# Kernel optimization log

Hardware: AMD Instinct MI355X
Metric: run time of the kernel (lower is better)

The kernel has to match this reference:

```python
import jax, jax.numpy as jnp
import numpy as np

N = 50000   # n_nodes (== input_dim, featureless identity features)
E = 800000  # edges per support (avg degree 16)
D = 200     # embed_dim (hardcoded in GIN)
C = 10      # num_classes


def setup_inputs() -> dict:
    key = jax.random.key(0)
    ks = jax.random.split(key, 8)
    x = jnp.zeros((N, 1), jnp.float32)  # unused: layer 0 is featureless
    rows0 = jax.random.randint(ks[0], (E,), 0, N, dtype=jnp.int32)
    cols0 = jax.random.randint(ks[1], (E,), 0, N, dtype=jnp.int32)
    vals0 = jax.random.uniform(ks[2], (E,), jnp.float32)
    rows1 = jax.random.randint(ks[3], (E,), 0, N, dtype=jnp.int32)
    cols1 = jax.random.randint(ks[4], (E,), 0, N, dtype=jnp.int32)
    vals1 = jax.random.uniform(ks[5], (E,), jnp.float32)
    W0 = jax.random.normal(ks[6], (N, D), jnp.float32) * 0.02
    W1 = jax.random.normal(ks[7], (D, C), jnp.float32) * 0.05
    eps0 = jnp.zeros((1,), jnp.float32)  # train_eps init (~1e-4 in repo)
    eps1 = jnp.zeros((1,), jnp.float32)
    return dict(x=x, rows0=rows0, cols0=cols0, vals0=vals0,
                rows1=rows1, cols1=cols1, vals1=vals1,
                W0=W0, W1=W1, eps0=eps0, eps1=eps1)


def reference(x, rows0, cols0, vals0, rows1, cols1, vals1, W0, W1, eps0, eps1):
    # sparse A @ X via gather + segment-sum (A in COO: rows, cols, vals)
    def spmm(r, c, v, X):
        return jax.ops.segment_sum(v[:, None] * X[c], r, num_segments=N)

    # Layer 0 (featureless, num_mlp_layers==1):
    #   AX = sum_i A_i ; out = AX @ W0 + 0.1*(1+eps0)*W0
    h0 = spmm(rows0, cols0, vals0, W0) + spmm(rows1, cols1, vals1, W0) \
         + 0.1 * (1.0 + eps0[0]) * W0
    h = jax.nn.relu(h0)  # [N, D]

    # Layer 1 (with features): out = (sum_i A_i @ h + 0.1*(1+eps1)*h) @ W1
    ax = spmm(rows0, cols0, vals0, h) + spmm(rows1, cols1, vals1, h)
    out = (ax + 0.1 * (1.0 + eps1[0]) * h) @ W1  # [N, C]
    return out
```

## Files before the change

kernel.cpp:

```cpp
#include <hip/hip_runtime.h>

#define N_NODES 50000
#define E_EDGES 800000
#define E2      (2 * E_EDGES)
#define D_DIM   200
#define C_CLS   10
#define NB_SCAN   ((N_NODES + 255) / 256)
#define NB_BUCKET ((N_NODES + 255) / 256)
#define BATCH     4096
#define CAP       12288

static __device__ __forceinline__ unsigned short f2bf(float f) {
    unsigned u = __float_as_uint(f);
    return (unsigned short)((u + 0x7FFFu + ((u >> 16) & 1u)) >> 16);
}
static __device__ __forceinline__ float bf_lo(unsigned u) {
    return __uint_as_float(u << 16);
}
static __device__ __forceinline__ float bf_hi(unsigned u) {
    return __uint_as_float(u & 0xFFFF0000u);
}

__global__ __launch_bounds__(256) void convert_w0_kernel(const float* __restrict__ W0,
                                                         unsigned short* __restrict__ W0h,
                                                         int* __restrict__ bcur) {
    if (blockIdx.x == 0 && threadIdx.x < NB_BUCKET) bcur[threadIdx.x] = 0;
    int i = (blockIdx.x * 256 + threadIdx.x) * 4;
    if (i >= N_NODES * D_DIM) return;
    float4 f = *(const float4*)(W0 + i);
    uint2 p;
    p.x = (unsigned)f2bf(f.x) | ((unsigned)f2bf(f.y) << 16);
    p.y = (unsigned)f2bf(f.z) | ((unsigned)f2bf(f.w) << 16);
    *(uint2*)(W0h + i) = p;
}

__global__ __launch_bounds__(256) void bucket_scatter_kernel(
        const int* __restrict__ rows0, const int* __restrict__ cols0,
        const float* __restrict__ vals0,
        const int* __restrict__ rows1, const int* __restrict__ cols1,
        const float* __restrict__ vals1,
        int* __restrict__ bcur,
        int2* __restrict__ stage) {
    __shared__ int cntL[NB_BUCKET];
    __shared__ int baseL[NB_BUCKET];
    __shared__ int offL[NB_BUCKET];
    __shared__ int2 recL[BATCH];
    const int tid = threadIdx.x;
    const int e0 = blockIdx.x * BATCH;

    for (int b = tid; b < NB_BUCKET; b += 256) cntL[b] = 0;
    __syncthreads();

#pragma unroll
    for (int k = 0; k < BATCH / 256; ++k) {
        int idx = k * 256 + tid;
        int e = e0 + idx;
        if (e < E2) {
            int r, c;
            float v;
            if (e < E_EDGES) {
                r = rows0[e]; c = cols0[e]; v = vals0[e];
            } else {
                int e1 = e - E_EDGES;
                r = rows1[e1]; c = cols1[e1]; v = vals1[e1];
            }
            recL[idx] = make_int2((int)((unsigned)r | ((unsigned)c << 16)),
                                  __float_as_int(v));
            atomicAdd(&cntL[r >> 8], 1);
        }
    }
    __syncthreads();

    for (int b = tid; b < NB_BUCKET; b += 256) {
        int c = cntL[b];
        baseL[b] = (c > 0) ? atomicAdd(&bcur[b], c) : 0;
        offL[b] = 0;
    }
    __syncthreads();

#pragma unroll
    for (int k = 0; k < BATCH / 256; ++k) {
        int idx = k * 256 + tid;
        int e = e0 + idx;
        if (e < E2) {
            int2 rec = recL[idx];
            int b = (int)(((unsigned)rec.x & 0xFFFFu) >> 8);
            int pos = baseL[b] + atomicAdd(&offL[b], 1);
            stage[(size_t)b * CAP + pos] = rec;
        }
    }
}

__global__ __launch_bounds__(256) void row_count_kernel(const int* __restrict__ bcur,
                                                        const int2* __restrict__ stage,
                                                        int* __restrict__ cnt) {
    __shared__ int hist[256];
    const int b = blockIdx.x;
    const int tid = threadIdx.x;
    hist[tid] = 0;
    __syncthreads();

    const int n = bcur[b];
    const int2* __restrict__ sp = stage + (size_t)b * CAP;
    for (int i = tid; i < n; i += 256)
        atomicAdd(&hist[(unsigned)sp[i].x & 255u], 1);
    __syncthreads();

    const int row = (b << 8) + tid;
    if (row < N_NODES) cnt[row] = hist[tid];
}

__global__ __launch_bounds__(256) void scan1_kernel(const int* __restrict__ cnt,
                                                    int* __restrict__ incl,
                                                    int* __restrict__ bsum) {
    const int i = blockIdx.x * 256 + threadIdx.x;
    const int lane = threadIdx.x & 63;
    const int w = threadIdx.x >> 6;
    int v = (i < N_NODES) ? cnt[i] : 0;
#pragma unroll
    for (int off = 1; off < 64; off <<= 1) {
        int t = __shfl_up(v, off, 64);
        if (lane >= off) v += t;
    }
    __shared__ int ws[4];
    if (lane == 63) ws[w] = v;
    __syncthreads();
    if (threadIdx.x == 0) {
        int s = 0;
#pragma unroll
        for (int k = 0; k < 4; ++k) { int t = ws[k]; ws[k] = s; s += t; }
    }
    __syncthreads();
    v += ws[w];
    if (i < N_NODES) incl[i] = v;
    if (threadIdx.x == 255) bsum[blockIdx.x] = v;
}

__global__ __launch_bounds__(64) void scan2_kernel(int* __restrict__ bsum,
                                                   int* __restrict__ row_ptr) {
    const int lane = threadIdx.x;
    int carry = 0;
    for (int base = 0; base < NB_SCAN; base += 64) {
        int idx = base + lane;
        int v = (idx < NB_SCAN) ? bsum[idx] : 0;
        int orig = v;
#pragma unroll
        for (int off = 1; off < 64; off <<= 1) {
            int t = __shfl_up(v, off, 64);
            if (lane >= off) v += t;
        }
        int chunk_total = __shfl(v, 63, 64);
        int excl = v - orig + carry;
        if (idx < NB_SCAN) bsum[idx] = excl;
        carry += chunk_total;
    }
    if (lane == 0) row_ptr[N_NODES] = carry;
}

__global__ __launch_bounds__(256) void scan3_kernel(const int* __restrict__ cnt,
                                                    const int* __restrict__ incl,
                                                    const int* __restrict__ bsum,
                                                    int* __restrict__ row_ptr) {
    int i = blockIdx.x * 256 + threadIdx.x;
    if (i >= N_NODES) return;
    row_ptr[i] = incl[i] - cnt[i] + bsum[blockIdx.x];
}

__global__ __launch_bounds__(256) void bucket_sort_kernel(
        const int* __restrict__ row_ptr,
        const int* __restrict__ bcur,
        const int2* __restrict__ stage,
        unsigned* __restrict__ cv4) {
    __shared__ int lcur[256];
    const int b = blockIdx.x;
    const int tid = threadIdx.x;
    const int row = (b << 8) + tid;
    lcur[tid] = (row < N_NODES) ? row_ptr[row] : 0;
    __syncthreads();

    const int n = bcur[b];
    const int2* __restrict__ sp = stage + (size_t)b * CAP;
    for (int i = tid; i < n; i += 256) {
        int2 rec = sp[i];
        unsigned u = (unsigned)rec.x;
        int pos = atomicAdd(&lcur[u & 255u], 1);
        cv4[pos] = (u & 0xFFFF0000u) | (unsigned)f2bf(__int_as_float(rec.y));
    }
}

__global__ __launch_bounds__(256) void spmm_layer0_fused_kernel(
        const int*  __restrict__ row_ptr,
        const unsigned* __restrict__ cv4,
        const unsigned short* __restrict__ W0h,
        const float* __restrict__ W1,
        const float* __restrict__ eps0,
        float* __restrict__ g) {
    __shared__ float W1s[D_DIM * C_CLS];
    for (int i = threadIdx.x; i < D_DIM * C_CLS; i += blockDim.x) W1s[i] = W1[i];
    __syncthreads();

    const int lane = threadIdx.x & 63;
    const int n = __builtin_amdgcn_readfirstlane(blockIdx.x * 4 + (threadIdx.x >> 6));
    if (n >= N_NODES) return;
    const float s0 = 0.1f * (1.0f + eps0[0]);
    const bool act = (lane < 50);
    const uint2* __restrict__ F = (const uint2*)W0h;

    const int beg  = row_ptr[n];
    const int endp = row_ptr[n + 1];
    float a0 = 0.f, a1 = 0.f, a2 = 0.f, a3 = 0.f;

    int e = beg;
    for (; e + 8 <= endp; e += 8) {
        unsigned w0 = cv4[e],     w1 = cv4[e + 1], w2 = cv4[e + 2], w3 = cv4[e + 3];
        unsigned w4 = cv4[e + 4], w5 = cv4[e + 5], w6 = cv4[e + 6], w7 = cv4[e + 7];
        if (act) {
            uint2 u0 = F[(size_t)(w0 >> 16) * 50 + lane];
            uint2 u1 = F[(size_t)(w1 >> 16) * 50 + lane];
            uint2 u2 = F[(size_t)(w2 >> 16) * 50 + lane];
            uint2 u3 = F[(size_t)(w3 >> 16) * 50 + lane];
            uint2 u4 = F[(size_t)(w4 >> 16) * 50 + lane];
            uint2 u5 = F[(size_t)(w5 >> 16) * 50 + lane];
            uint2 u6 = F[(size_t)(w6 >> 16) * 50 + lane];
            uint2 u7 = F[(size_t)(w7 >> 16) * 50 + lane];
            float v0 = __uint_as_float(w0 << 16), v1 = __uint_as_float(w1 << 16);
            float v2 = __uint_as_float(w2 << 16), v3 = __uint_as_float(w3 << 16);
            float v4 = __uint_as_float(w4 << 16), v5 = __uint_as_float(w5 << 16);
            float v6 = __uint_as_float(w6 << 16), v7 = __uint_as_float(w7 << 16);
            a0 += v0 * bf_lo(u0.x) + v1 * bf_lo(u1.x) + v2 * bf_lo(u2.x) + v3 * bf_lo(u3.x)
                + v4 * bf_lo(u4.x) + v5 * bf_lo(u5.x) + v6 * bf_lo(u6.x) + v7 * bf_lo(u7.x);
            a1 += v0 * bf_hi(u0.x) + v1 * bf_hi(u1.x) + v2 * bf_hi(u2.x) + v3 * bf_hi(u3.x)
                + v4 * bf_hi(u4.x) + v5 * bf_hi(u5.x) + v6 * bf_hi(u6.x) + v7 * bf_hi(u7.x);
            a2 += v0 * bf_lo(u0.y) + v1 * bf_lo(u1.y) + v2 * bf_lo(u2.y) + v3 * bf_lo(u3.y)
                + v4 * bf_lo(u4.y) + v5 * bf_lo(u5.y) + v6 * bf_lo(u6.y) + v7 * bf_lo(u7.y);
            a3 += v0 * bf_hi(u0.y) + v1 * bf_hi(u1.y) + v2 * bf_hi(u2.y) + v3 * bf_hi(u3.y)
                + v4 * bf_hi(u4.y) + v5 * bf_hi(u5.y) + v6 * bf_hi(u6.y) + v7 * bf_hi(u7.y);
        }
    }
    for (; e + 4 <= endp; e += 4) {
        unsigned w0 = cv4[e], w1 = cv4[e + 1], w2 = cv4[e + 2], w3 = cv4[e + 3];
        if (act) {
            uint2 u0 = F[(size_t)(w0 >> 16) * 50 + lane];
            uint2 u1 = F[(size_t)(w1 >> 16) * 50 + lane];
            uint2 u2 = F[(size_t)(w2 >> 16) * 50 + lane];
            uint2 u3 = F[(size_t)(w3 >> 16) * 50 + lane];
            float v0 = __uint_as_float(w0 << 16), v1 = __uint_as_float(w1 << 16);
            float v2 = __uint_as_float(w2 << 16), v3 = __uint_as_float(w3 << 16);
            a0 += v0 * bf_lo(u0.x) + v1 * bf_lo(u1.x) + v2 * bf_lo(u2.x) + v3 * bf_lo(u3.x);
            a1 += v0 * bf_hi(u0.x) + v1 * bf_hi(u1.x) + v2 * bf_hi(u2.x) + v3 * bf_hi(u3.x);
            a2 += v0 * bf_lo(u0.y) + v1 * bf_lo(u1.y) + v2 * bf_lo(u2.y) + v3 * bf_lo(u3.y);
            a3 += v0 * bf_hi(u0.y) + v1 * bf_hi(u1.y) + v2 * bf_hi(u2.y) + v3 * bf_hi(u3.y);
        }
    }
    for (; e < endp; ++e) {
        unsigned w = cv4[e];
        if (act) {
            uint2 u = F[(size_t)(w >> 16) * 50 + lane];
            float v = __uint_as_float(w << 16);
            a0 += v * bf_lo(u.x);
            a1 += v * bf_hi(u.x);
            a2 += v * bf_lo(u.y);
            a3 += v * bf_hi(u.y);
        }
    }

    float o[C_CLS];
#pragma unroll
    for (int k = 0; k < C_CLS; ++k) o[k] = 0.f;

    if (act) {
        uint2 w = F[(size_t)n * 50 + lane];
        a0 = fmaxf(a0 + s0 * bf_lo(w.x), 0.f);
        a1 = fmaxf(a1 + s0 * bf_hi(w.x), 0.f);
        a2 = fmaxf(a2 + s0 * bf_lo(w.y), 0.f);
        a3 = fmaxf(a3 + s0 * bf_hi(w.y), 0.f);
        const int d = lane * 4;
#pragma unroll
        for (int k = 0; k < C_CLS; ++k) {
            o[k] = a0 * W1s[(d + 0) * C_CLS + k]
                 + a1 * W1s[(d + 1) * C_CLS + k]
                 + a2 * W1s[(d + 2) * C_CLS + k]
                 + a3 * W1s[(d + 3) * C_CLS + k];
        }
    }

#pragma unroll
    for (int k = 0; k < C_CLS; ++k) {
        for (int off = 32; off > 0; off >>= 1)
            o[k] += __shfl_xor(o[k], off, 64);
    }

    if (lane == 0) {
        float* gp = g + (size_t)n * C_CLS;
#pragma unroll
        for (int k = 0; k < C_CLS; ++k) gp[k] = o[k];
    }
}

__global__ __launch_bounds__(256) void spmm_layer1_light_kernel(
        const int*  __restrict__ row_ptr,
        const unsigned* __restrict__ cv4,
        const float* __restrict__ g,
        const float* __restrict__ eps1,
        float* __restrict__ out) {
    const int lane = threadIdx.x & 63;
    const int n = __builtin_amdgcn_readfirstlane(blockIdx.x * 4 + (threadIdx.x >> 6));
    if (n >= N_NODES) return;
    const int grp = lane / 10;
    const int d   = lane - grp * 10;
    const float s1 = 0.1f * (1.0f + eps1[0]);

    const int beg  = row_ptr[n];
    const int endp = row_ptr[n + 1];
    float acc = 0.f;

    for (int base = beg; base < endp; base += 6) {
        int e = base + grp;
        if (grp < 6 && e < endp) {
            unsigned p = cv4[e];
            float vf = __uint_as_float(p << 16);
            acc += vf * g[(size_t)(p >> 16) * C_CLS + d];
        }
    }

    float t;
    t = __shfl(acc, lane + 10, 64); if (lane < 50) acc += t;
    t = __shfl(acc, lane + 20, 64); if (lane < 30) acc += t;
    t = __shfl(acc, lane + 40, 64); if (lane < 10) acc += t;

    if (lane < 10) {
        out[(size_t)n * C_CLS + d] = acc + s1 * g[(size_t)n * C_CLS + d];
    }
}

extern "C" void kernel_launch(void* const* d_in, const int* in_sizes, int n_in,
                              void* d_out, int out_size, void* d_ws, size_t ws_size,
                              hipStream_t stream) {
    const int*   rows0 = (const int*)d_in[1];
    const int*   cols0 = (const int*)d_in[2];
    const float* vals0 = (const float*)d_in[3];
    const int*   rows1 = (const int*)d_in[4];
    const int*   cols1 = (const int*)d_in[5];
    const float* vals1 = (const float*)d_in[6];
    const float* W0    = (const float*)d_in[7];
    const float* W1    = (const float*)d_in[8];
    const float* eps0  = (const float*)d_in[9];
    const float* eps1  = (const float*)d_in[10];
    float* out = (float*)d_out;

    char* ws = (char*)d_ws;
    size_t off = 0;
    auto alloc = [&](size_t bytes) {
        void* p = ws + off;
        off += (bytes + 255) & ~(size_t)255;
        return p;
    };
    unsigned short* W0h = (unsigned short*)alloc((size_t)N_NODES * D_DIM * 2);
    float* g      = (float*)alloc((size_t)N_NODES * C_CLS * 4);
    int* cnt      = (int*)alloc((size_t)N_NODES * 4);
    int* incl     = (int*)alloc((size_t)N_NODES * 4);
    int* bsum     = (int*)alloc((size_t)NB_SCAN * 4);
    int* row_ptr  = (int*)alloc((size_t)(N_NODES + 1) * 4);
    int* bcur     = (int*)alloc((size_t)NB_BUCKET * 4);
    unsigned* cv4 = (unsigned*)alloc((size_t)E2 * 4);
    int2* stage   = (int2*)alloc((size_t)NB_BUCKET * CAP * 8);
    (void)ws_size;

    convert_w0_kernel<<<(N_NODES * D_DIM / 4 + 255) / 256, 256, 0, stream>>>(W0, W0h, bcur);
    bucket_scatter_kernel<<<(E2 + BATCH - 1) / BATCH, 256, 0, stream>>>(
        rows0, cols0, vals0, rows1, cols1, vals1, bcur, stage);
    row_count_kernel<<<NB_BUCKET, 256, 0, stream>>>(bcur, stage, cnt);
    scan1_kernel<<<NB_SCAN, 256, 0, stream>>>(cnt, incl, bsum);
    scan2_kernel<<<1, 64, 0, stream>>>(bsum, row_ptr);
    scan3_kernel<<<NB_SCAN, 256, 0, stream>>>(cnt, incl, bsum, row_ptr);
    bucket_sort_kernel<<<NB_BUCKET, 256, 0, stream>>>(row_ptr, bcur, stage, cv4);

    const int spmm_grid = (N_NODES + 3) / 4;
    spmm_layer0_fused_kernel<<<spmm_grid, 256, 0, stream>>>(
        row_ptr, cv4, W0h, W1, eps0, g);
    spmm_layer1_light_kernel<<<spmm_grid, 256, 0, stream>>>(
        row_ptr, cv4, g, eps1, out);
}
```

Baseline: 283.4 us.

## Fuse row histogram with block scan and fold final scan into sort placement

Merges the row-count and first-level scan kernels into one per-bucket kernel, and folds the scan3 offset addition into the sort placement kernel, cutting the CSR build from five kernels to three and removing the cnt/incl intermediate arrays. Bucket reservations are also padded to multiples of 8 and filled with sentinel records, which the consumers skip. This cuts launches and global round-trips in the preprocessing chain, at the cost of extra sentinel writes and per-record sentinel checks.

```diff
diff --git a/kernel.cpp b/kernel.cpp
--- a/kernel.cpp
+++ b/kernel.cpp
@@ -5,10 +5,10 @@
 #define E2      (2 * E_EDGES)
 #define D_DIM   200
 #define C_CLS   10
-#define NB_SCAN   ((N_NODES + 255) / 256)
 #define NB_BUCKET ((N_NODES + 255) / 256)
 #define BATCH     4096
 #define CAP       12288
+#define SENT      0xFFFFu
 
 static __device__ __forceinline__ unsigned short f2bf(float f) {
     unsigned u = __float_as_uint(f);
@@ -73,8 +73,13 @@
 
     for (int b = tid; b < NB_BUCKET; b += 256) {
         int c = cntL[b];
-        baseL[b] = (c > 0) ? atomicAdd(&bcur[b], c) : 0;
+        int cpad = (c + 7) & ~7;
+        int base = (cpad > 0) ? atomicAdd(&bcur[b], cpad) : 0;
+        baseL[b] = base;
         offL[b] = 0;
+        int2* bp = stage + (size_t)b * CAP;
+        for (int s = base + c; s < base + cpad; ++s)
+            bp[s] = make_int2((int)SENT, 0);
     }
     __syncthreads();
 
@@ -91,58 +96,57 @@
     }
 }
 
-__global__ __launch_bounds__(256) void row_count_kernel(const int* __restrict__ bcur,
+__global__ __launch_bounds__(256) void hist_scan_kernel(const int* __restrict__ bcur,
                                                         const int2* __restrict__ stage,
-                                                        int* __restrict__ cnt) {
+                                                        int* __restrict__ excl,
+                                                        int* __restrict__ bsum) {
     __shared__ int hist[256];
+    __shared__ int ws4[4];
     const int b = blockIdx.x;
     const int tid = threadIdx.x;
+    const int lane = tid & 63;
+    const int w = tid >> 6;
     hist[tid] = 0;
     __syncthreads();
 
     const int n = bcur[b];
     const int2* __restrict__ sp = stage + (size_t)b * CAP;
-    for (int i = tid; i < n; i += 256)
-        atomicAdd(&hist[(unsigned)sp[i].x & 255u], 1);
-    __syncthreads();
-
-    const int row = (b << 8) + tid;
-    if (row < N_NODES) cnt[row] = hist[tid];
-}
-
-__global__ __launch_bounds__(256) void scan1_kernel(const int* __restrict__ cnt,
-                                                    int* __restrict__ incl,
-                                                    int* __restrict__ bsum) {
-    const int i = blockIdx.x * 256 + threadIdx.x;
-    const int lane = threadIdx.x & 63;
-    const int w = threadIdx.x >> 6;
-    int v = (i < N_NODES) ? cnt[i] : 0;
+    for (int i = tid; i < n; i += 256) {
+        unsigned u = (unsigned)sp[i].x;
+        if ((u & 0xFFFFu) != SENT)
+            atomicAdd(&hist[u & 255u], 1);
+    }
+    __syncthreads();
+
+    int v = hist[tid];
+    int orig = v;
 #pragma unroll
     for (int off = 1; off < 64; off <<= 1) {
         int t = __shfl_up(v, off, 64);
         if (lane >= off) v += t;
     }
-    __shared__ int ws[4];
-    if (lane == 63) ws[w] = v;
-    __syncthreads();
-    if (threadIdx.x == 0) {
+    if (lane == 63) ws4[w] = v;
+    __syncthreads();
+    if (tid == 0) {
         int s = 0;
 #pragma unroll
-        for (int k = 0; k < 4; ++k) { int t = ws[k]; ws[k] = s; s += t; }
-    }
-    __syncthreads();
-    v += ws[w];
-    if (i < N_NODES) incl[i] = v;
-    if (threadIdx.x == 255) bsum[blockIdx.x] = v;
+        for (int k = 0; k < 4; ++k) { int t = ws4[k]; ws4[k] = s; s += t; }
+    }
+    __syncthreads();
+    v += ws4[w];
+
+    const int row = (b << 8) + tid;
+    if (row < N_NODES) excl[row] = v - orig;
+    if (tid == 255) bsum[b] = v;
 }
 
 __global__ __launch_bounds__(64) void scan2_kernel(int* __restrict__ bsum,
                                                    int* __restrict__ row_ptr) {
     const int lane = threadIdx.x;
     int carry = 0;
-    for (int base = 0; base < NB_SCAN; base += 64) {
+    for (int base = 0; base < NB_BUCKET; base += 64) {
         int idx = base + lane;
-        int v = (idx < NB_SCAN) ? bsum[idx] : 0;
+        int v = (idx < NB_BUCKET) ? bsum[idx] : 0;
         int orig = v;
 #pragma unroll
         for (int off = 1; off < 64; off <<= 1) {
@@ -150,32 +154,27 @@
             if (lane >= off) v += t;
         }
         int chunk_total = __shfl(v, 63, 64);
-        int excl = v - orig + carry;
-        if (idx < NB_SCAN) bsum[idx] = excl;
+        int ex = v - orig + carry;
+        if (idx < NB_BUCKET) bsum[idx] = ex;
         carry += chunk_total;
     }
     if (lane == 0) row_ptr[N_NODES] = carry;
 }
 
-__global__ __launch_bounds__(256) void scan3_kernel(const int* __restrict__ cnt,
-                                                    const int* __restrict__ incl,
-                                                    const int* __restrict__ bsum,
-                                                    int* __restrict__ row_ptr) {
-    int i = blockIdx.x * 256 + threadIdx.x;
-    if (i >= N_NODES) return;
-    row_ptr[i] = incl[i] - cnt[i] + bsum[blockIdx.x];
-}
-
-__global__ __launch_bounds__(256) void bucket_sort_kernel(
-        const int* __restrict__ row_ptr,
-        const int* __restrict__ bcur,
-        const int2* __restrict__ stage,
-        unsigned* __restrict__ cv4) {
+__global__ __launch_bounds__(256) void sort_place_kernel(const int* __restrict__ excl,
+                                                         const int* __restrict__ bsum,
+                                                         const int* __restrict__ bcur,
+                                                         const int2* __restrict__ stage,
+                                                         int* __restrict__ row_ptr,
+                                                         unsigned* __restrict__ cv4) {
     __shared__ int lcur[256];
     const int b = blockIdx.x;
     const int tid = threadIdx.x;
+    const int base = bsum[b];
     const int row = (b << 8) + tid;
-    lcur[tid] = (row < N_NODES) ? row_ptr[row] : 0;
+    int ex = base + ((row < N_NODES) ? excl[row] : 0);
+    if (row < N_NODES) row_ptr[row] = ex;
+    lcur[tid] = ex;
     __syncthreads();
 
     const int n = bcur[b];
@@ -183,6 +182,7 @@
     for (int i = tid; i < n; i += 256) {
         int2 rec = sp[i];
         unsigned u = (unsigned)rec.x;
+        if ((u & 0xFFFFu) == SENT) continue;
         int pos = atomicAdd(&lcur[u & 255u], 1);
         cv4[pos] = (u & 0xFFFF0000u) | (unsigned)f2bf(__int_as_float(rec.y));
     }
@@ -357,9 +357,8 @@
     };
     unsigned short* W0h = (unsigned short*)alloc((size_t)N_NODES * D_DIM * 2);
     float* g      = (float*)alloc((size_t)N_NODES * C_CLS * 4);
-    int* cnt      = (int*)alloc((size_t)N_NODES * 4);
-    int* incl     = (int*)alloc((size_t)N_NODES * 4);
-    int* bsum     = (int*)alloc((size_t)NB_SCAN * 4);
+    int* excl     = (int*)alloc((size_t)N_NODES * 4);
+    int* bsum     = (int*)alloc((size_t)NB_BUCKET * 4);
     int* row_ptr  = (int*)alloc((size_t)(N_NODES + 1) * 4);
     int* bcur     = (int*)alloc((size_t)NB_BUCKET * 4);
     unsigned* cv4 = (unsigned*)alloc((size_t)E2 * 4);
@@ -369,11 +368,9 @@
     convert_w0_kernel<<<(N_NODES * D_DIM / 4 + 255) / 256, 256, 0, stream>>>(W0, W0h, bcur);
     bucket_scatter_kernel<<<(E2 + BATCH - 1) / BATCH, 256, 0, stream>>>(
         rows0, cols0, vals0, rows1, cols1, vals1, bcur, stage);
-    row_count_kernel<<<NB_BUCKET, 256, 0, stream>>>(bcur, stage, cnt);
-    scan1_kernel<<<NB_SCAN, 256, 0, stream>>>(cnt, incl, bsum);
+    hist_scan_kernel<<<NB_BUCKET, 256, 0, stream>>>(bcur, stage, excl, bsum);
     scan2_kernel<<<1, 64, 0, stream>>>(bsum, row_ptr);
-    scan3_kernel<<<NB_SCAN, 256, 0, stream>>>(cnt, incl, bsum, row_ptr);
-    bucket_sort_kernel<<<NB_BUCKET, 256, 0, stream>>>(row_ptr, bcur, stage, cv4);
+    sort_place_kernel<<<NB_BUCKET, 256, 0, stream>>>(excl, bsum, bcur, stage, row_ptr, cv4);
 
     const int spmm_grid = (N_NODES + 3) / 4;
     spmm_layer0_fused_kernel<<<spmm_grid, 256, 0, stream>>>(
```

Result: no change. 287.1 us (+1.3%).
